# Performance work log

Measured on AMD Instinct MI355X. Metric: run time of the kernel, lower is better.

Reference implementation:

```python
import jax, jax.numpy as jnp
import numpy as np

T_PAD, C_PAD = 8, 8   # padded LUT dims (Liberty LUTs are <=8x8 here)
EPS = 1e-12


def _sorted_table(key, n, m):
    # strictly increasing per-row breakpoint tables
    steps = jax.random.uniform(key, (n, m), minval=0.01, maxval=1.0, dtype=jnp.float32)
    return jnp.cumsum(steps, axis=1)


def _interp_all(x_t, x_c, vals, t_tbl, c_tbl, td, cd):
    """Vectorized LUT lookup: scalar / 1D-trans / 1D-cap / 2D bilinear, masked.
    x_t,x_c: [B]; vals: [B, T*C]; t_tbl: [B,T]; c_tbl: [B,C]; td,cd: [B] int.
    """
    B = x_t.shape[0]
    rows = jnp.arange(B)
    ss = jax.vmap(lambda tbl, x: jnp.searchsorted(tbl, x, side='right'))
    max_t = jnp.maximum(td - 1, 0)
    max_c = jnp.maximum(cd - 1, 0)
    # clamp(min=1) then clamp(max=actual-1), matching torch sequential clamps
    t_hi = jnp.minimum(jnp.maximum(ss(t_tbl, x_t), 1), max_t)
    c_hi = jnp.minimum(jnp.maximum(ss(c_tbl, x_c), 1), max_c)
    t_lo = jnp.maximum(t_hi - 1, 0)
    c_lo = jnp.maximum(c_hi - 1, 0)
    t0 = t_tbl[rows, t_lo]; t1 = t_tbl[rows, t_hi]
    c0 = c_tbl[rows, c_lo]; c1 = c_tbl[rows, c_hi]
    ti = t1 - t0; ci = c1 - c0
    t_deg = jnp.abs(ti) < EPS
    c_deg = jnp.abs(ci) < EPS
    xt = jnp.clip(x_t, t0, t1)
    xc = jnp.clip(x_c, c0, c1)
    ti_s = jnp.where(t_deg, EPS, ti)
    ci_s = jnp.where(c_deg, EPS, ci)
    ft = jnp.clip((xt - t0) / ti_s, 0.0, 1.0)
    fc = jnp.clip((xc - c0) / ci_s, 0.0, 1.0)
    # ---- 2D bilinear (row-major with ACTUAL cap-dim stride, as in torch code)
    v00 = vals[rows, t_lo * cd + c_lo]
    v01 = vals[rows, t_lo * cd + c_hi]
    v10 = vals[rows, t_hi * cd + c_lo]
    v11 = vals[rows, t_hi * cd + c_hi]
    wa = (t1 - xt) * (c1 - xc)
    wb = (t1 - xt) * (xc - c0)
    wc_ = (xt - t0) * (c1 - xc)
    wd = (xt - t0) * (xc - c0)
    bil = (v00 * wa + v01 * wb + v10 * wc_ + v11 * wd) / (ti_s * ci_s)
    val2d = jnp.where(t_deg & c_deg, v00,
            jnp.where(t_deg, v00 + (v01 - v00) * fc,
            jnp.where(c_deg, v00 + (v10 - v00) * ft, bil)))
    # ---- 1D over trans (cap dim <= 1 -> values row is effectively [T])
    y0t = vals[rows, t_lo]; y1t = vals[rows, t_hi]
    val1t = jnp.where(t_deg, y0t, y0t + (y1t - y0t) * ft)
    # ---- 1D over cap (trans dim <= 1 -> values row is effectively [C])
    y0c = vals[rows, c_lo]; y1c = vals[rows, c_hi]
    val1c = jnp.where(c_deg, y0c, y0c + (y1c - y0c) * fc)
    # ---- scalar
    val_s = vals[rows, 0]
    is2d = (td > 1) & (cd > 1)
    is1t = (td > 1) & (cd <= 1)
    is1c = (td <= 1) & (cd > 1)
    valid = (td > 0) & (cd > 0)
    out = jnp.where(is2d, val2d,
          jnp.where(is1t, val1t,
          jnp.where(is1c, val1c, val_s)))
    return jnp.where(valid, out, jnp.zeros_like(out))


def setup_inputs() -> dict:
    N_ARCS, B = 500_000, 2_000_000
    k = jax.random.key(0)
    k1, k2, k3, k4, k5, k6, k7 = jax.random.split(k, 7)
    trans_tbl = _sorted_table(k1, N_ARCS, T_PAD)        # [N, 8] sorted
    cap_tbl = _sorted_table(k2, N_ARCS, C_PAD)          # [N, 8] sorted
    values = jax.random.normal(k3, (N_ARCS, T_PAD * C_PAD), dtype=jnp.float32)
    dims = jax.random.randint(k4, (N_ARCS, 2), 0, T_PAD + 1, dtype=jnp.int32)
    arc_idxs = jax.random.randint(k5, (B,), 0, N_ARCS, dtype=jnp.int32)
    input_trans = jax.random.uniform(k6, (B,), minval=0.0, maxval=9.0, dtype=jnp.float32)
    output_caps = jax.random.uniform(k7, (B,), minval=0.0, maxval=9.0, dtype=jnp.float32)
    return {
        'input_trans': input_trans,
        'output_caps': output_caps,
        'arc_idxs': arc_idxs,
        'flat_luts_values': values,
        'flat_luts_trans_table': trans_tbl,
        'flat_luts_cap_table': cap_tbl,
        'flat_luts_dim': dims,
    }


def reference(input_trans, output_caps, arc_idxs, flat_luts_values,
              flat_luts_trans_table, flat_luts_cap_table, flat_luts_dim):
    # per-eval gather of LUT rows (the irregular-access hot spot)
    vals = flat_luts_values[arc_idxs]          # [B, 64]
    t_tbl = flat_luts_trans_table[arc_idxs]    # [B, 8]
    c_tbl = flat_luts_cap_table[arc_idxs]      # [B, 8]
    td = flat_luts_dim[arc_idxs, 0]
    cd = flat_luts_dim[arc_idxs, 1]
    return _interp_all(input_trans, output_caps, vals, t_tbl, c_tbl, td, cd)
```

## Files before the change

### kernel.cpp

```cpp
#include <hip/hip_runtime.h>

#define EPS 1e-12f

__device__ __forceinline__ float sel8(const float4& a, const float4& b, int i) {
    float lo = (i == 0) ? a.x : (i == 1) ? a.y : (i == 2) ? a.z : a.w;
    float hi = (i == 4) ? b.x : (i == 5) ? b.y : (i == 6) ? b.z : b.w;
    return (i < 4) ? lo : hi;
}

__global__ __launch_bounds__(256) void TimingPropagation_35622458753425_kernel(
    const float* __restrict__ x_t_arr,
    const float* __restrict__ x_c_arr,
    const int*   __restrict__ arcs,
    const float* __restrict__ values,
    const float* __restrict__ t_table,
    const float* __restrict__ c_table,
    const int*   __restrict__ dims,
    float*       __restrict__ out,
    int B)
{
    int i = blockIdx.x * blockDim.x + threadIdx.x;
    if (i >= B) return;

    float x_t = x_t_arr[i];
    float x_c = x_c_arr[i];
    int arc = arcs[i];

    const int2 d = ((const int2*)dims)[arc];
    const int td = d.x, cd = d.y;

    const float4* tt = (const float4*)(t_table + (size_t)arc * 8);
    float4 ta = tt[0], tb = tt[1];
    const float4* ct = (const float4*)(c_table + (size_t)arc * 8);
    float4 ca = ct[0], cb = ct[1];

    int ss_t = (ta.x <= x_t) + (ta.y <= x_t) + (ta.z <= x_t) + (ta.w <= x_t)
             + (tb.x <= x_t) + (tb.y <= x_t) + (tb.z <= x_t) + (tb.w <= x_t);
    int ss_c = (ca.x <= x_c) + (ca.y <= x_c) + (ca.z <= x_c) + (ca.w <= x_c)
             + (cb.x <= x_c) + (cb.y <= x_c) + (cb.z <= x_c) + (cb.w <= x_c);

    int max_t = max(td - 1, 0);
    int max_c = max(cd - 1, 0);
    int t_hi = min(max(ss_t, 1), max_t);
    int c_hi = min(max(ss_c, 1), max_c);
    int t_lo = max(t_hi - 1, 0);
    int c_lo = max(c_hi - 1, 0);

    float t0 = sel8(ta, tb, t_lo), t1 = sel8(ta, tb, t_hi);
    float c0 = sel8(ca, cb, c_lo), c1 = sel8(ca, cb, c_hi);

    float ti = t1 - t0, ci = c1 - c0;
    float xt = fminf(fmaxf(x_t, t0), t1);
    float xc = fminf(fmaxf(x_c, c0), c1);
    float ti_s = (fabsf(ti) < EPS) ? EPS : ti;
    float ci_s = (fabsf(ci) < EPS) ? EPS : ci;
    float ft = fminf(fmaxf((xt - t0) / ti_s, 0.f), 1.f);
    float fc = fminf(fmaxf((xc - c0) / ci_s, 0.f), 1.f);

    bool is2d = (td > 1) && (cd > 1);
    bool is1t = (td > 1) && (cd <= 1);
    bool is1c = (td <= 1) && (cd > 1);
    bool valid = (td > 0) && (cd > 0);

    int i00 = is2d ? (t_lo * cd + c_lo) : is1t ? t_lo : is1c ? c_lo : 0;
    int i01 = is2d ? (t_lo * cd + c_hi) : is1c ? c_hi : i00;
    int i10 = is2d ? (t_hi * cd + c_lo) : is1t ? t_hi : i00;
    int i11 = is2d ? (t_hi * cd + c_hi) : i00;

    const float* vrow = values + (size_t)arc * 64;
    float v00 = vrow[i00];
    float v01 = vrow[i01];
    float v10 = vrow[i10];
    float v11 = vrow[i11];

    float wa = (t1 - xt) * (c1 - xc);
    float wb = (t1 - xt) * (xc - c0);
    float wc = (xt - t0) * (c1 - xc);
    float wd = (xt - t0) * (xc - c0);
    float bil = (v00 * wa + v01 * wb + v10 * wc + v11 * wd) / (ti_s * ci_s);

    float lin_t = v00 + (v10 - v00) * ft;
    float lin_c = v00 + (v01 - v00) * fc;

    float r = is2d ? bil : is1t ? lin_t : is1c ? lin_c : v00;
    out[i] = valid ? r : 0.0f;
}

extern "C" void kernel_launch(void* const* d_in, const int* in_sizes, int n_in,
                              void* d_out, int out_size, void* d_ws, size_t ws_size,
                              hipStream_t stream) {
    const float* x_t   = (const float*)d_in[0];
    const float* x_c   = (const float*)d_in[1];
    const int*   arcs  = (const int*)d_in[2];
    const float* vals  = (const float*)d_in[3];
    const float* t_tbl = (const float*)d_in[4];
    const float* c_tbl = (const float*)d_in[5];
    const int*   dims  = (const int*)d_in[6];
    float* out = (float*)d_out;
    int B = in_sizes[0];
    int block = 256;
    int grid = (B + block - 1) / block;
    TimingPropagation_35622458753425_kernel<<<grid, block, 0, stream>>>(
        x_t, x_c, arcs, vals, t_tbl, c_tbl, dims, out, B);
}
```

Before: 315.0 us.

## Bucket-sort evaluations by arc before LUT lookup to localize gathers

Adds a counting-sort pipeline (histogram, scan, atomic scatter) that groups evaluations by high bits of the arc index into a workspace payload, then runs the LUT interpolation over the sorted order and scatters results back. The aim is to make the LUT row gathers spatially coherent so cache lines are reused. In exchange it adds four extra launches, a memset, global atomics, an extra read/write pass over the payload, and a scattered output write. The original single kernel remains as a fallback when the workspace is too small.

```diff
diff --git a/kernel.cpp b/kernel.cpp
--- a/kernel.cpp
+++ b/kernel.cpp
@@ -1,6 +1,7 @@
 #include <hip/hip_runtime.h>
 
 #define EPS 1e-12f
+#define NB 4096
 
 __device__ __forceinline__ float sel8(const float4& a, const float4& b, int i) {
     float lo = (i == 0) ? a.x : (i == 1) ? a.y : (i == 2) ? a.z : a.w;
@@ -8,24 +9,11 @@
     return (i < 4) ? lo : hi;
 }
 
-__global__ __launch_bounds__(256) void TimingPropagation_35622458753425_kernel(
-    const float* __restrict__ x_t_arr,
-    const float* __restrict__ x_c_arr,
-    const int*   __restrict__ arcs,
-    const float* __restrict__ values,
-    const float* __restrict__ t_table,
-    const float* __restrict__ c_table,
-    const int*   __restrict__ dims,
-    float*       __restrict__ out,
-    int B)
-{
-    int i = blockIdx.x * blockDim.x + threadIdx.x;
-    if (i >= B) return;
-
-    float x_t = x_t_arr[i];
-    float x_c = x_c_arr[i];
-    int arc = arcs[i];
-
+__device__ __forceinline__ float lut_eval(int arc, float x_t, float x_c,
+                                          const float* __restrict__ values,
+                                          const float* __restrict__ t_table,
+                                          const float* __restrict__ c_table,
+                                          const int*   __restrict__ dims) {
     const int2 d = ((const int2*)dims)[arc];
     const int td = d.x, cd = d.y;
 
@@ -83,7 +71,85 @@
     float lin_c = v00 + (v01 - v00) * fc;
 
     float r = is2d ? bil : is1t ? lin_t : is1c ? lin_c : v00;
-    out[i] = valid ? r : 0.0f;
+    return valid ? r : 0.0f;
+}
+
+__global__ __launch_bounds__(256) void TimingPropagation_35622458753425_kernel(
+    const float* __restrict__ x_t_arr, const float* __restrict__ x_c_arr,
+    const int* __restrict__ arcs, const float* __restrict__ values,
+    const float* __restrict__ t_table, const float* __restrict__ c_table,
+    const int* __restrict__ dims, float* __restrict__ out, int B)
+{
+    int i = blockIdx.x * blockDim.x + threadIdx.x;
+    if (i >= B) return;
+    out[i] = lut_eval(arcs[i], x_t_arr[i], x_c_arr[i], values, t_table, c_table, dims);
+}
+
+__global__ __launch_bounds__(1024) void k_hist(const int* __restrict__ arcs, int B,
+                                               int shift, unsigned* __restrict__ hist) {
+    __shared__ unsigned lh[NB];
+    for (int v = threadIdx.x; v < NB; v += blockDim.x) lh[v] = 0;
+    __syncthreads();
+    int stride = gridDim.x * blockDim.x;
+    for (int i = blockIdx.x * blockDim.x + threadIdx.x; i < B; i += stride)
+        atomicAdd(&lh[((unsigned)arcs[i]) >> shift], 1u);
+    __syncthreads();
+    for (int v = threadIdx.x; v < NB; v += blockDim.x) {
+        unsigned c = lh[v];
+        if (c) atomicAdd(&hist[v], c);
+    }
+}
+
+__global__ __launch_bounds__(1024) void k_scan(const unsigned* __restrict__ hist,
+                                               unsigned* __restrict__ cursor) {
+    __shared__ unsigned part[1024];
+    int t = threadIdx.x;
+    unsigned h0 = hist[4 * t], h1 = hist[4 * t + 1], h2 = hist[4 * t + 2], h3 = hist[4 * t + 3];
+    unsigned s = h0 + h1 + h2 + h3;
+    part[t] = s;
+    __syncthreads();
+    for (int off = 1; off < 1024; off <<= 1) {
+        unsigned v = (t >= off) ? part[t - off] : 0u;
+        __syncthreads();
+        part[t] += v;
+        __syncthreads();
+    }
+    unsigned excl = part[t] - s;
+    cursor[4 * t]     = excl;
+    cursor[4 * t + 1] = excl + h0;
+    cursor[4 * t + 2] = excl + h0 + h1;
+    cursor[4 * t + 3] = excl + h0 + h1 + h2;
+}
+
+__global__ __launch_bounds__(256) void k_scatter(const float* __restrict__ xt,
+                                                 const float* __restrict__ xc,
+                                                 const int* __restrict__ arcs, int B,
+                                                 int shift, unsigned* __restrict__ cursor,
+                                                 float4* __restrict__ pay) {
+    int i = blockIdx.x * blockDim.x + threadIdx.x;
+    if (i >= B) return;
+    int a = arcs[i];
+    unsigned pos = atomicAdd(&cursor[((unsigned)a) >> shift], 1u);
+    float4 p;
+    p.x = xt[i];
+    p.y = xc[i];
+    p.z = __int_as_float(a);
+    p.w = __int_as_float(i);
+    pay[pos] = p;
+}
+
+__global__ __launch_bounds__(256) void k_compute(const float4* __restrict__ pay, int B,
+                                                 const float* __restrict__ values,
+                                                 const float* __restrict__ t_table,
+                                                 const float* __restrict__ c_table,
+                                                 const int* __restrict__ dims,
+                                                 float* __restrict__ out) {
+    int j = blockIdx.x * blockDim.x + threadIdx.x;
+    if (j >= B) return;
+    float4 p = pay[j];
+    int arc = __float_as_int(p.z);
+    int i   = __float_as_int(p.w);
+    out[i] = lut_eval(arc, p.x, p.y, values, t_table, c_table, dims);
 }
 
 extern "C" void kernel_launch(void* const* d_in, const int* in_sizes, int n_in,
@@ -98,8 +164,27 @@
     const int*   dims  = (const int*)d_in[6];
     float* out = (float*)d_out;
     int B = in_sizes[0];
-    int block = 256;
-    int grid = (B + block - 1) / block;
-    TimingPropagation_35622458753425_kernel<<<grid, block, 0, stream>>>(
-        x_t, x_c, arcs, vals, t_tbl, c_tbl, dims, out, B);
+    int N = in_sizes[3] / 64;
+
+    size_t need = 32 * 1024 + (size_t)B * 16;
+    if (ws_size < need) {
+        int grid = (B + 255) / 256;
+        TimingPropagation_35622458753425_kernel<<<grid, 256, 0, stream>>>(
+            x_t, x_c, arcs, vals, t_tbl, c_tbl, dims, out, B);
+        return;
+    }
+
+    int shift = 0;
+    while ((((unsigned)(N - 1)) >> shift) >= NB) shift++;
+
+    unsigned* hist   = (unsigned*)d_ws;
+    unsigned* cursor = (unsigned*)((char*)d_ws + 16 * 1024);
+    float4*   pay    = (float4*)((char*)d_ws + 32 * 1024);
+
+    hipMemsetAsync(hist, 0, NB * sizeof(unsigned), stream);
+    k_hist<<<128, 1024, 0, stream>>>(arcs, B, shift, hist);
+    k_scan<<<1, 1024, 0, stream>>>(hist, cursor);
+    int grid = (B + 255) / 256;
+    k_scatter<<<grid, 256, 0, stream>>>(x_t, x_c, arcs, B, shift, cursor, pay);
+    k_compute<<<grid, 256, 0, stream>>>(pay, B, vals, t_tbl, c_tbl, dims, out);
 }
```

New measurement: 423.4 us. +34.4%, slower.

## Repack trans/cap tables into one 64-byte record per arc and compress dims to bytes

Applied to the files above, without the earlier changes.

Adds a pre-pass kernel that interleaves each arc's trans and cap breakpoint tables into a single contiguous 64-byte record, and packs the two dims into one byte per arc in workspace. The main kernel then gathers one record per evaluation instead of touching two separate table rows plus an 8-byte dims entry, which aims to cut scattered cache-line traffic. The cost is an extra launch and a full pass over all arcs on every call. If N is large relative to B, that extra pass may outweigh what the gather saves.

```diff
diff --git a/kernel.cpp b/kernel.cpp
--- a/kernel.cpp
+++ b/kernel.cpp
@@ -8,32 +8,10 @@
     return (i < 4) ? lo : hi;
 }
 
-__global__ __launch_bounds__(256) void TimingPropagation_35622458753425_kernel(
-    const float* __restrict__ x_t_arr,
-    const float* __restrict__ x_c_arr,
-    const int*   __restrict__ arcs,
-    const float* __restrict__ values,
-    const float* __restrict__ t_table,
-    const float* __restrict__ c_table,
-    const int*   __restrict__ dims,
-    float*       __restrict__ out,
-    int B)
-{
-    int i = blockIdx.x * blockDim.x + threadIdx.x;
-    if (i >= B) return;
-
-    float x_t = x_t_arr[i];
-    float x_c = x_c_arr[i];
-    int arc = arcs[i];
-
-    const int2 d = ((const int2*)dims)[arc];
-    const int td = d.x, cd = d.y;
-
-    const float4* tt = (const float4*)(t_table + (size_t)arc * 8);
-    float4 ta = tt[0], tb = tt[1];
-    const float4* ct = (const float4*)(c_table + (size_t)arc * 8);
-    float4 ca = ct[0], cb = ct[1];
-
+__device__ __forceinline__ float lut_eval_core(int arc, float x_t, float x_c,
+                                               int td, int cd,
+                                               float4 ta, float4 tb, float4 ca, float4 cb,
+                                               const float* __restrict__ values) {
     int ss_t = (ta.x <= x_t) + (ta.y <= x_t) + (ta.z <= x_t) + (ta.w <= x_t)
              + (tb.x <= x_t) + (tb.y <= x_t) + (tb.z <= x_t) + (tb.w <= x_t);
     int ss_c = (ca.x <= x_c) + (ca.y <= x_c) + (ca.z <= x_c) + (ca.w <= x_c)
@@ -83,7 +61,79 @@
     float lin_c = v00 + (v01 - v00) * fc;
 
     float r = is2d ? bil : is1t ? lin_t : is1c ? lin_c : v00;
-    out[i] = valid ? r : 0.0f;
+    return valid ? r : 0.0f;
+}
+
+__global__ __launch_bounds__(256) void k_repack(const float* __restrict__ t_table,
+                                                const float* __restrict__ c_table,
+                                                const int* __restrict__ dims,
+                                                float4* __restrict__ packed,
+                                                unsigned char* __restrict__ dims8,
+                                                int N) {
+    int a = blockIdx.x * blockDim.x + threadIdx.x;
+    if (a >= N) return;
+    const float4* tt = (const float4*)(t_table + (size_t)a * 8);
+    const float4* cc = (const float4*)(c_table + (size_t)a * 8);
+    float4* dst = packed + (size_t)a * 4;
+    dst[0] = tt[0];
+    dst[1] = tt[1];
+    dst[2] = cc[0];
+    dst[3] = cc[1];
+    if (dims8) {
+        int2 d = ((const int2*)dims)[a];
+        dims8[a] = (unsigned char)((d.x & 0xF) | ((d.y & 0xF) << 4));
+    }
+}
+
+__global__ __launch_bounds__(256) void k_main_d8(
+    const float* __restrict__ x_t_arr, const float* __restrict__ x_c_arr,
+    const int* __restrict__ arcs, const float* __restrict__ values,
+    const float4* __restrict__ packed, const unsigned char* __restrict__ dims8,
+    float* __restrict__ out, int B)
+{
+    int i = blockIdx.x * blockDim.x + threadIdx.x;
+    if (i >= B) return;
+    float x_t = x_t_arr[i];
+    float x_c = x_c_arr[i];
+    int arc = arcs[i];
+    unsigned char dp = dims8[arc];
+    int td = dp & 0xF, cd = dp >> 4;
+    const float4* rec = packed + (size_t)arc * 4;
+    float4 ta = rec[0], tb = rec[1], ca = rec[2], cb = rec[3];
+    out[i] = lut_eval_core(arc, x_t, x_c, td, cd, ta, tb, ca, cb, values);
+}
+
+__global__ __launch_bounds__(256) void k_main_d32(
+    const float* __restrict__ x_t_arr, const float* __restrict__ x_c_arr,
+    const int* __restrict__ arcs, const float* __restrict__ values,
+    const float4* __restrict__ packed, const int* __restrict__ dims,
+    float* __restrict__ out, int B)
+{
+    int i = blockIdx.x * blockDim.x + threadIdx.x;
+    if (i >= B) return;
+    float x_t = x_t_arr[i];
+    float x_c = x_c_arr[i];
+    int arc = arcs[i];
+    int2 d = ((const int2*)dims)[arc];
+    const float4* rec = packed + (size_t)arc * 4;
+    float4 ta = rec[0], tb = rec[1], ca = rec[2], cb = rec[3];
+    out[i] = lut_eval_core(arc, x_t, x_c, d.x, d.y, ta, tb, ca, cb, values);
+}
+
+__global__ __launch_bounds__(256) void TimingPropagation_35622458753425_kernel(
+    const float* __restrict__ x_t_arr, const float* __restrict__ x_c_arr,
+    const int* __restrict__ arcs, const float* __restrict__ values,
+    const float* __restrict__ t_table, const float* __restrict__ c_table,
+    const int* __restrict__ dims, float* __restrict__ out, int B)
+{
+    int i = blockIdx.x * blockDim.x + threadIdx.x;
+    if (i >= B) return;
+    int arc = arcs[i];
+    int2 d = ((const int2*)dims)[arc];
+    const float4* tt = (const float4*)(t_table + (size_t)arc * 8);
+    const float4* cc = (const float4*)(c_table + (size_t)arc * 8);
+    float4 ta = tt[0], tb = tt[1], ca = cc[0], cb = cc[1];
+    out[i] = lut_eval_core(arc, x_t_arr[i], x_c_arr[i], d.x, d.y, ta, tb, ca, cb, values);
 }
 
 extern "C" void kernel_launch(void* const* d_in, const int* in_sizes, int n_in,
@@ -98,8 +148,25 @@
     const int*   dims  = (const int*)d_in[6];
     float* out = (float*)d_out;
     int B = in_sizes[0];
-    int block = 256;
-    int grid = (B + block - 1) / block;
-    TimingPropagation_35622458753425_kernel<<<grid, block, 0, stream>>>(
-        x_t, x_c, arcs, vals, t_tbl, c_tbl, dims, out, B);
+    int N = in_sizes[3] / 64;
+
+    size_t need_tc = (size_t)N * 64;
+    size_t need_d8 = need_tc + (size_t)N;
+
+    int gridB = (B + 255) / 256;
+    int gridN = (N + 255) / 256;
+
+    if (ws_size >= need_d8) {
+        float4* packed = (float4*)d_ws;
+        unsigned char* dims8 = (unsigned char*)d_ws + need_tc;
+        k_repack<<<gridN, 256, 0, stream>>>(t_tbl, c_tbl, dims, packed, dims8, N);
+        k_main_d8<<<gridB, 256, 0, stream>>>(x_t, x_c, arcs, vals, packed, dims8, out, B);
+    } else if (ws_size >= need_tc) {
+        float4* packed = (float4*)d_ws;
+        k_repack<<<gridN, 256, 0, stream>>>(t_tbl, c_tbl, dims, packed, nullptr, N);
+        k_main_d32<<<gridB, 256, 0, stream>>>(x_t, x_c, arcs, vals, packed, dims, out, B);
+    } else {
+        TimingPropagation_35622458753425_kernel<<<gridB, 256, 0, stream>>>(
+            x_t, x_c, arcs, vals, t_tbl, c_tbl, dims, out, B);
+    }
 }
```

Result: faster. 292.9 us (-7.0%).
